# Kernel optimization log

Measured on AMD Instinct MI355X. Metric: run time of the kernel, lower is better.

The kernel has to match this reference:

```python
import jax, jax.numpy as jnp
import numpy as np

B, S, D_MODEL, H = 2, 2048, 1024, 16
HD = D_MODEL // H  # 64


def rotate_half(x):
    # pairs (x_even, x_odd) -> (-x_odd, x_even), interleaved back
    x1 = x[..., ::2]
    x2 = x[..., 1::2]
    return jnp.stack([-x2, x1], axis=-1).reshape(x.shape)


def rope_sin_cos(seq_len, head_dim):
    pos = jnp.arange(seq_len, dtype=jnp.float32)
    dim = jnp.arange(head_dim, dtype=jnp.float32)
    theta = 10000.0 ** (-2.0 * jnp.floor(dim / 2.0) / head_dim)
    angles = pos[:, None] * theta[None, :]  # [S, HD]
    return jnp.sin(angles), jnp.cos(angles)


def setup_inputs():
    key = jax.random.key(0)
    ks = jax.random.split(key, 6)
    w_scale = 1.0 / np.sqrt(D_MODEL)
    x = jax.random.normal(ks[0], (B, S, D_MODEL), jnp.float32)
    # causal mask: 1.0 where attention is disallowed (j > i)
    mask = (1.0 - jnp.tril(jnp.ones((S, S), jnp.float32)))[None, None, :, :]
    wq = jax.random.normal(ks[1], (D_MODEL, D_MODEL), jnp.float32) * w_scale
    wk = jax.random.normal(ks[2], (D_MODEL, D_MODEL), jnp.float32) * w_scale
    wv = jax.random.normal(ks[3], (D_MODEL, D_MODEL), jnp.float32) * w_scale
    wo = jax.random.normal(ks[4], (D_MODEL, D_MODEL), jnp.float32) * w_scale
    zeros = jnp.zeros((D_MODEL,), jnp.float32)
    return dict(x=x, mask=mask, wq=wq, bq=zeros, wk=wk, bk=zeros,
                wv=wv, bv=zeros, wo=wo, bo=zeros)


def reference(x, mask, wq, bq, wk, bk, wv, bv, wo, bo):
    b, s, _ = x.shape

    def split_heads(t):  # [B,S,D] -> [B,H,S,HD]
        return t.reshape(b, s, H, HD).transpose(0, 2, 1, 3)

    q = split_heads(x @ wq + bq)
    k = split_heads(x @ wk + bk)
    v = split_heads(x @ wv + bv)

    sin, cos = rope_sin_cos(s, HD)
    sin = sin[None, None, :, :]
    cos = cos[None, None, :, :]
    q = q * cos + rotate_half(q) * sin
    k = k * cos + rotate_half(k) * sin

    logits = jnp.einsum('bhqd,bhkd->bhqk', q, k) / jnp.sqrt(jnp.float32(HD))
    logits = logits + mask * (-1e9)
    attn = jax.nn.softmax(logits, axis=-1)
    out = jnp.einsum('bhqk,bhkd->bhqd', attn, v)  # [B,H,S,HD]
    out = out.transpose(0, 2, 1, 3).reshape(b, s, D_MODEL)
    return out @ wo + bo
```

## Files before the change

kernel.cpp:

```cpp
#include <hip/hip_runtime.h>
#include <hip/hip_bf16.h>


#define S_ 2048
#define DM 1024
#define HD 64

typedef __attribute__((ext_vector_type(8))) short short8;
typedef __attribute__((ext_vector_type(4))) float floatx4;

__device__ __forceinline__ unsigned short f2b(float x) {
  union { __hip_bfloat16 h; unsigned short u; } cv;
  cv.h = __float2bfloat16(x);
  return cv.u;
}

__device__ __forceinline__ unsigned cvt_pk_bf16(float lo, float hi) {
  unsigned r;
  asm("v_cvt_pk_bf16_f32 %0, %1, %2" : "=v"(r) : "v"(lo), "v"(hi));
  return r;
}

__device__ __forceinline__ void gload_lds16(const unsigned short* g, unsigned short* l) {
  typedef const __attribute__((address_space(1))) unsigned int* gp_t;
  typedef __attribute__((address_space(3))) unsigned int* lp_t;
  __builtin_amdgcn_global_load_lds((gp_t)(const void*)g, (lp_t)(void*)l, 16, 0, 0);
}

__global__ void prep_kernel(const float* __restrict__ x,
                            const float* __restrict__ w0, const float* __restrict__ w1,
                            const float* __restrict__ w2, const float* __restrict__ w3,
                            unsigned short* __restrict__ xc,
                            unsigned short* __restrict__ wt,
                            float2* __restrict__ rope) {
  const int bid = blockIdx.x;
  if (bid < 4096) {
    int i = (bid * 256 + threadIdx.x) * 4;
    float4 v = *(const float4*)(x + i);
    ushort4 o;
    o.x = f2b(v.x); o.y = f2b(v.y); o.z = f2b(v.z); o.w = f2b(v.w);
    *(ushort4*)(xc + i) = o;
  } else if (bid < 8192) {
    __shared__ float tile[32][33];
    const int rem = bid - 4096;
    const int z = rem >> 10;
    const int bx = (rem & 1023) & 31;
    const int by = (rem & 1023) >> 5;
    const float* W = (z == 0) ? w0 : (z == 1) ? w1 : (z == 2) ? w2 : w3;
    unsigned short* Wt = wt + (size_t)z * DM * DM;
    const int tx = threadIdx.x & 31;
    const int ty = threadIdx.x >> 5;
    const int k0 = bx * 32;
    const int c0 = by * 32;
#pragma unroll
    for (int i = 0; i < 4; ++i)
      tile[ty + i * 8][tx] = W[(size_t)(k0 + ty + i * 8) * DM + c0 + tx];
    __syncthreads();
#pragma unroll
    for (int i = 0; i < 4; ++i)
      Wt[(size_t)(c0 + ty + i * 8) * DM + k0 + tx] = f2b(tile[tx][ty + i * 8]);
  } else {
    int i = (bid - 8192) * 256 + threadIdx.x;
    int s = i >> 5, d2 = i & 31;
    float th = expf(-(float)d2 * (9.210340371976184f / 32.0f));
    float sn, cs;
    sincosf((float)s * th, &sn, &cs);
    rope[i] = make_float2(cs, sn);
  }
}

__global__ __launch_bounds__(256, 4) void gemm_qkv(
    const unsigned short* __restrict__ A, const unsigned short* __restrict__ Wt,
    const float* __restrict__ bq, const float* __restrict__ bk,
    const float* __restrict__ bv, const float2* __restrict__ rope,
    unsigned short* __restrict__ QKV) {
  __shared__ __attribute__((aligned(16))) unsigned short As[128 * 64];
  __shared__ __attribute__((aligned(16))) unsigned short Bs[64 * 64];
  const int r0 = blockIdx.x * 128;
  const int c0 = blockIdx.y * 64;
  const int t = threadIdx.x;
  const int lane = t & 63;
  const int wv = t >> 6;
  const int wr = (wv >> 1) * 64;
  const int wc = (wv & 1) * 32;
  const int lr = lane & 15;
  const int lg = lane >> 4;

  const int chunk = lane >> 3;
  const int sseg = ((lane & 7) ^ chunk) * 8;
  const unsigned short* Ag = A + (size_t)(r0 + wv * 32 + chunk) * DM + sseg;
  const unsigned short* Bg = Wt + (size_t)(c0 + wv * 16 + chunk) * DM + sseg;
  unsigned short* lA = &As[wv * 32 * 64];
  unsigned short* lB = &Bs[wv * 16 * 64];

  floatx4 acc[4][2] = {};
  const int fswz = (lr & 7) << 4;

  for (int k0 = 0; k0 < DM; k0 += 64) {
#pragma unroll
    for (int j = 0; j < 4; ++j)
      gload_lds16(Ag + k0 + j * 8 * DM, lA + j * 8 * 64);
#pragma unroll
    for (int j = 0; j < 2; ++j)
      gload_lds16(Bg + k0 + j * 8 * DM, lB + j * 8 * 64);
    __syncthreads();
#pragma unroll
    for (int kk = 0; kk < 2; ++kk) {
      short8 af[4], bf[2];
#pragma unroll
      for (int m = 0; m < 4; ++m)
        af[m] = *(const short8*)((char*)As + (wr + m * 16 + lr) * 128 +
                                 ((kk * 64 + lg * 16) ^ fswz));
#pragma unroll
      for (int n = 0; n < 2; ++n)
        bf[n] = *(const short8*)((char*)Bs + (wc + n * 16 + lr) * 128 +
                                 ((kk * 64 + lg * 16) ^ fswz));
#pragma unroll
      for (int m = 0; m < 4; ++m)
#pragma unroll
        for (int n = 0; n < 2; ++n)
          acc[m][n] = __builtin_amdgcn_mfma_f32_16x16x32_bf16(af[m], bf[n], acc[m][n], 0, 0, 0);
    }
    __syncthreads();
  }

  const int mat = blockIdx.y >> 4;
  const float* bias = (mat == 0) ? bq : (mat == 1) ? bk : bv;
  const int rbase = r0 + wr + lg * 4;
  const int cbase = c0 + wc + lr;
#pragma unroll
  for (int n = 0; n < 2; ++n) {
    const int c = cbase + n * 16;
    const int cc = c & (DM - 1);
    const float bvv = bias[cc];
    const int d = c & 63;
    const int h = cc >> 6;
#pragma unroll
    for (int m = 0; m < 4; ++m) {
#pragma unroll
      for (int i = 0; i < 4; ++i) {
        const int r = rbase + m * 16 + i;
        const int s = r & (S_ - 1);
        const int b = r >> 11;
        float v = acc[m][n][i] + bvv;
        float pv = __shfl_xor(v, 1);
        if (mat < 2) {
          float2 cssn = rope[s * 32 + (d >> 1)];
          v = (d & 1) ? fmaf(v, cssn.x, pv * cssn.y) : fmaf(v, cssn.x, -pv * cssn.y);
          if (mat == 0) v *= 0.18033688011112042f;
        }
        QKV[((size_t)((mat << 5) | (b << 4) | h) * S_ + s) * HD + d] = f2b(v);
      }
    }
  }
}

__global__ __launch_bounds__(256, 4) void gemm_out(
    const unsigned short* __restrict__ A, const unsigned short* __restrict__ Wt,
    const float* __restrict__ bias, float* __restrict__ out) {
  __shared__ __attribute__((aligned(16))) unsigned short As[64 * 64];
  __shared__ __attribute__((aligned(16))) unsigned short Bs[64 * 64];
  const int r0 = blockIdx.x * 64;
  const int c0 = blockIdx.y * 64;
  const int t = threadIdx.x;
  const int lane = t & 63;
  const int wv = t >> 6;
  const int wr = (wv >> 1) * 32;
  const int wc = (wv & 1) * 32;
  const int lr = lane & 15;
  const int lg = lane >> 4;

  const int chunk = lane >> 3;
  const int sseg = ((lane & 7) ^ chunk) * 8;
  const unsigned short* Ag = A + (size_t)(r0 + wv * 8 + chunk) * DM + sseg;
  const unsigned short* Bg = Wt + (size_t)(c0 + wv * 8 + chunk) * DM + sseg;
  unsigned short* lA = &As[wv * 8 * 64];
  unsigned short* lB = &Bs[wv * 8 * 64];

  floatx4 acc[2][2] = {};
  const int fswz = (lr & 7) << 4;

  for (int k0 = 0; k0 < DM; k0 += 64) {
#pragma unroll
    for (int j = 0; j < 2; ++j) {
      gload_lds16(Ag + k0 + j * 32 * DM, lA + j * 32 * 64);
      gload_lds16(Bg + k0 + j * 32 * DM, lB + j * 32 * 64);
    }
    __syncthreads();
#pragma unroll
    for (int kk = 0; kk < 2; ++kk) {
      short8 af[2], bf[2];
#pragma unroll
      for (int m = 0; m < 2; ++m)
        af[m] = *(const short8*)((char*)As + (wr + m * 16 + lr) * 128 +
                                 ((kk * 64 + lg * 16) ^ fswz));
#pragma unroll
      for (int n = 0; n < 2; ++n)
        bf[n] = *(const short8*)((char*)Bs + (wc + n * 16 + lr) * 128 +
                                 ((kk * 64 + lg * 16) ^ fswz));
#pragma unroll
      for (int m = 0; m < 2; ++m)
#pragma unroll
        for (int n = 0; n < 2; ++n)
          acc[m][n] = __builtin_amdgcn_mfma_f32_16x16x32_bf16(af[m], bf[n], acc[m][n], 0, 0, 0);
    }
    __syncthreads();
  }

  const int rbase = r0 + wr + lg * 4;
  const int cbase = c0 + wc + lr;
#pragma unroll
  for (int n = 0; n < 2; ++n) {
    const int c = cbase + n * 16;
    const float bvv = bias[c];
#pragma unroll
    for (int m = 0; m < 2; ++m) {
#pragma unroll
      for (int i = 0; i < 4; ++i) {
        const int r = rbase + m * 16 + i;
        out[(size_t)r * DM + c] = acc[m][n][i] + bvv;
      }
    }
  }
}

#define ATTN_STEP(TT, BUF, KLA, KLB)                                           \
  do {                                                                         \
    {                  \
      char* Vb = (char*)Vs[BUF];                                               \
      const unsigned* ua = (const unsigned*)&va;                               \
      const unsigned* ub = (const unsigned*)&vb;                               \
      _Pragma("unroll") for (int j = 0; j < 8; ++j) {                          \
        unsigned pkv = __builtin_amdgcn_perm(                                  \
            ub[j >> 1], ua[j >> 1], (j & 1) ? 0x07060302u : 0x05040100u);      \
        *(unsigned*)(Vb + (oct * 8 + j) * 128 + ((4 * kp) ^ (j << 4))) = pkv;  \
      }                                                                        \
    }                                                                          \
    if ((TT) < qt) {                                \
      va = *(const short8*)(Vpref);                                            \
      vb = *(const short8*)(Vpref + 64);                                       \
      Vpref += 4096;                                                           \
    }                                                                          \
                        \
    asm volatile("s_waitcnt lgkmcnt(0)" ::: "memory");                         \
    __builtin_amdgcn_s_barrier();                                              \
                 \
    if ((TT) < qt) asm volatile("s_waitcnt vmcnt(2)" ::: "memory");            \
    else           asm volatile("s_waitcnt vmcnt(0)" ::: "memory");            \
    __builtin_amdgcn_sched_barrier(0);                                         \
    if ((TT) < qt) {                   \
      gload_lds16(Kpref, KLA);                                                 \
      gload_lds16(Kpref + 2048, KLB);                                          \
      Kpref += 4096;                                                           \
    }                                                                          \
                     \
    floatx4 s[4] = {};                                                         \
    __builtin_amdgcn_s_setprio(1);                                             \
    _Pragma("unroll") for (int kk = 0; kk < 2; ++kk) {                         \
      _Pragma("unroll") for (int n = 0; n < 4; ++n) {                          \
        int r = n * 16 + lr;                                                   \
        short8 kf = *(const short8*)((char*)Ks[BUF] + r * 128 +                \
                                     ((kk * 64 + lg * 16) ^ ((r & 7) << 4)));  \
        s[n] = __builtin_amdgcn_mfma_f32_16x16x32_bf16(kf, qf[kk], s[n], 0, 0, 0); \
      }                                                                        \
    }                                                                          \
    __builtin_amdgcn_s_setprio(0);                                             \
    if ((TT) == qt) {                                                          \
      _Pragma("unroll") for (int n = 0; n < 4; ++n)                            \
        _Pragma("unroll") for (int i = 0; i < 4; ++i)                          \
          if (n * 16 + lg * 4 + i > qin) s[n][i] = -1e30f;                     \
    }                                                                          \
                              \
    float ta = fmaxf(fmaxf(s[0][0], s[0][1]), s[0][2]);                        \
    float tb = fmaxf(fmaxf(s[0][3], s[1][0]), s[1][1]);                        \
    float tc = fmaxf(fmaxf(s[1][2], s[1][3]), s[2][0]);                        \
    float td = fmaxf(fmaxf(s[2][1], s[2][2]), s[2][3]);                        \
    float te = fmaxf(fmaxf(s[3][0], s[3][1]), s[3][2]);                        \
    float tm = fmaxf(fmaxf(ta, tb), tc);                                       \
    tm = fmaxf(fmaxf(tm, td), te);                                             \
    tm = fmaxf(tm, s[3][3]);                                                   \
              \
    if (__any(tm > m + 8.f)) {                                                 \
      tm = fmaxf(tm, __shfl_xor(tm, 16));                                      \
      tm = fmaxf(tm, __shfl_xor(tm, 32));                                      \
      const float mn = fmaxf(m, tm);                                           \
      const float al = exp2f(m - mn);                                          \
      m = mn;                                                                  \
      lsum *= al;                                                              \
      _Pragma("unroll") for (int dd = 0; dd < 4; ++dd) o[dd] *= al;            \
    }                                                                          \
    float ps = 0.f;                                                            \
    _Pragma("unroll") for (int n = 0; n < 4; ++n) {                            \
      _Pragma("unroll") for (int i = 0; i < 4; ++i) {                          \
        float p = exp2f(s[n][i] - m);                                          \
        s[n][i] = p;                                                           \
        ps += p;                                                               \
      }                                                                        \
    }                                                                          \
    lsum += ps;                                                                \
                         \
    _Pragma("unroll") for (int n = 0; n < 4; ++n) {                            \
      _Pragma("unroll") for (int hh = 0; hh < 2; ++hh) {                       \
        unsigned pk = cvt_pk_bf16(s[n][2 * hh], s[n][2 * hh + 1]);             \
        *(unsigned*)(Pw + lr * 128 +                                           \
                     (((n * 16 + lg * 4 + 2 * hh) * 2) ^ pswz)) = pk;          \
      }                                                                        \
    }                                                                          \
    short8 pb[2];                                                              \
    _Pragma("unroll") for (int kk = 0; kk < 2; ++kk)                           \
      pb[kk] = *(const short8*)(Pw + lr * 128 + ((kk * 64 + lg * 16) ^ pswz)); \
    __builtin_amdgcn_s_setprio(1);                                             \
    _Pragma("unroll") for (int kk = 0; kk < 2; ++kk)                           \
      _Pragma("unroll") for (int dd = 0; dd < 4; ++dd) {                       \
        int d = dd * 16 + lr;                                                  \
        short8 vbf = *(const short8*)((char*)Vs[BUF] + d * 128 +               \
                                      ((kk * 64 + lg * 16) ^ ((d & 7) << 4))); \
        o[dd] = __builtin_amdgcn_mfma_f32_16x16x32_bf16(vbf, pb[kk], o[dd], 0, 0, 0); \
      }                                                                        \
    __builtin_amdgcn_s_setprio(0);                                             \
  } while (0)

__global__ __launch_bounds__(256, 4) void attn_kernel(
    const unsigned short* __restrict__ Q, const unsigned short* __restrict__ K,
    const unsigned short* __restrict__ V, unsigned short* __restrict__ AttnC) {
  __shared__ __attribute__((aligned(16))) unsigned short Ks[2][64 * 64];
  __shared__ __attribute__((aligned(16))) unsigned short Vs[2][64 * 64];
  __shared__ __attribute__((aligned(16))) unsigned short Ps[4][16 * 64];

  const int bh = blockIdx.x;
  const int qt = 31 - (int)blockIdx.y;
  const int tid = threadIdx.x;
  const int w = tid >> 6;
  const int l = tid & 63;
  const int lg = l >> 4;
  const int lr = l & 15;
  const size_t base = (size_t)bh * S_ * HD;
  const int qin = w * 16 + lr;

  short8 qf[2];
  {
    const unsigned short* Qrow =
        Q + base + (size_t)(qt * 64 + w * 16 + lr) * HD + lg * 8;
    qf[0] = *(const short8*)(Qrow);
    qf[1] = *(const short8*)(Qrow + 32);
  }

  floatx4 o[4] = {};
  float m = -1e30f, lsum = 0.f;

  const int krow = tid >> 3;
  const int kseg = tid & 7;
  const unsigned short* Kpref = K + base + krow * 64 + ((kseg ^ (krow & 7)) * 8);
  unsigned short* const kld0a = &Ks[0][w * 512];
  unsigned short* const kld0b = &Ks[0][2048 + w * 512];
  unsigned short* const kld1a = &Ks[1][w * 512];
  unsigned short* const kld1b = &Ks[1][2048 + w * 512];

  const int oct = tid >> 5;
  const int kp = tid & 31;
  const unsigned short* Vpref = V + base + 2 * kp * 64 + oct * 8;

  short8 va = *(const short8*)(Vpref);
  short8 vb = *(const short8*)(Vpref + 64);
  Vpref += 4096;
  gload_lds16(Kpref, kld0a);
  gload_lds16(Kpref + 2048, kld0b);
  Kpref += 4096;

  char* const Pw = (char*)Ps[w];
  const int pswz = (lr & 7) << 4;

  int t = 0;
#pragma unroll 1
  for (; t + 1 <= qt; t += 2) {
    ATTN_STEP(t, 0, kld1a, kld1b);
    ATTN_STEP(t + 1, 1, kld0a, kld0b);
  }
  if (t <= qt) ATTN_STEP(t, 0, kld1a, kld1b);

  lsum += __shfl_xor(lsum, 16);
  lsum += __shfl_xor(lsum, 32);
  const float inv = 1.f / lsum;
  unsigned short* orow =
      AttnC + (size_t)((bh >> 4) * S_ + qt * 64 + w * 16 + lr) * DM + (bh & 15) * HD;
#pragma unroll
  for (int dd = 0; dd < 4; ++dd) {
    unsigned w0 = cvt_pk_bf16(o[dd][0] * inv, o[dd][1] * inv);
    unsigned w1 = cvt_pk_bf16(o[dd][2] * inv, o[dd][3] * inv);
    *(uint2*)(orow + dd * 16 + lg * 4) = make_uint2(w0, w1);
  }
}

extern "C" void kernel_launch(void* const* d_in, const int* in_sizes, int n_in,
                              void* d_out, int out_size, void* d_ws, size_t ws_size,
                              hipStream_t stream) {
  const float* x = (const float*)d_in[0];
  const float* wq = (const float*)d_in[2];
  const float* bq = (const float*)d_in[3];
  const float* wk = (const float*)d_in[4];
  const float* bk = (const float*)d_in[5];
  const float* wv = (const float*)d_in[6];
  const float* bv = (const float*)d_in[7];
  const float* wo = (const float*)d_in[8];
  const float* bo = (const float*)d_in[9];

  char* ws = (char*)d_ws;
  const size_t MB = 1024ull * 1024ull;
  unsigned short* Xc = (unsigned short*)(ws);
  unsigned short* Wt = (unsigned short*)(ws + 8 * MB);
  unsigned short* QKVb = (unsigned short*)(ws + 16 * MB);
  unsigned short* Ac = (unsigned short*)(ws + 40 * MB);
  float2* rope = (float2*)(ws + 48 * MB);

  prep_kernel<<<8448, 256, 0, stream>>>(x, wq, wk, wv, wo, Xc, Wt, rope);
  gemm_qkv<<<dim3(32, 48), 256, 0, stream>>>(Xc, Wt, bq, bk, bv, rope, QKVb);
  attn_kernel<<<dim3(32, 32), 256, 0, stream>>>(
      QKVb, QKVb + 32ull * S_ * HD, QKVb + 64ull * S_ * HD, Ac);
  gemm_out<<<dim3(64, 16), 256, 0, stream>>>(Ac, Wt + 3ull * DM * DM, bo, (float*)d_out);
}
```

Before: 106.0 us.

## Write V transposed from QKV GEMM and load it via async LDS copies

The QKV GEMM epilogue for the V matrix now stages the tile in shared memory and writes V transposed ([b,h,d,s]) to a separate buffer. The attention kernel then fetches V^T tiles with direct global-to-LDS loads, the same way it fetches K, instead of loading V into registers and transposing it with byte permutes and LDS stores each step. This removes per-step register transposes and LDS write traffic in the attention inner loop. In exchange the GEMM epilogue gains an extra shared-memory pass and barrier, and the attention prologue now waits for the first tiles before entering the loop.

Measured after the change: 105.3 us, median of 2. About the same (-0.6%).

```diff
diff --git a/kernel.cpp b/kernel.cpp
--- a/kernel.cpp
+++ b/kernel.cpp
@@ -73,8 +73,8 @@
     const unsigned short* __restrict__ A, const unsigned short* __restrict__ Wt,
     const float* __restrict__ bq, const float* __restrict__ bk,
     const float* __restrict__ bv, const float2* __restrict__ rope,
-    unsigned short* __restrict__ QKV) {
-  __shared__ __attribute__((aligned(16))) unsigned short As[128 * 64];
+    unsigned short* __restrict__ QKV, unsigned short* __restrict__ VT) {
+  __shared__ __attribute__((aligned(16))) unsigned short As[64 * 136];
   __shared__ __attribute__((aligned(16))) unsigned short Bs[64 * 64];
   const int r0 = blockIdx.x * 128;
   const int c0 = blockIdx.y * 64;
@@ -128,28 +128,53 @@
   const float* bias = (mat == 0) ? bq : (mat == 1) ? bk : bv;
   const int rbase = r0 + wr + lg * 4;
   const int cbase = c0 + wc + lr;
-#pragma unroll
-  for (int n = 0; n < 2; ++n) {
-    const int c = cbase + n * 16;
-    const int cc = c & (DM - 1);
-    const float bvv = bias[cc];
-    const int d = c & 63;
-    const int h = cc >> 6;
-#pragma unroll
-    for (int m = 0; m < 4; ++m) {
-#pragma unroll
-      for (int i = 0; i < 4; ++i) {
-        const int r = rbase + m * 16 + i;
-        const int s = r & (S_ - 1);
-        const int b = r >> 11;
-        float v = acc[m][n][i] + bvv;
-        float pv = __shfl_xor(v, 1);
-        if (mat < 2) {
+
+  if (mat == 2) {
+    unsigned short* Ls = As;
+#pragma unroll
+    for (int n = 0; n < 2; ++n) {
+      const int dl = wc + n * 16 + lr;
+      const float bvv = bias[(c0 & (DM - 1)) + dl];
+#pragma unroll
+      for (int m = 0; m < 4; ++m)
+#pragma unroll
+        for (int i = 0; i < 4; ++i)
+          Ls[dl * 136 + (wr + m * 16 + lg * 4 + i)] = f2b(acc[m][n][i] + bvv);
+    }
+    __syncthreads();
+    const int b2 = r0 >> 11;
+    const int h2 = (c0 & (DM - 1)) >> 6;
+    const int s0 = r0 & (S_ - 1);
+    unsigned short* VTb = VT + ((size_t)((b2 << 4) | h2) * 64) * S_ + s0;
+#pragma unroll
+    for (int j = 0; j < 4; ++j) {
+      const int idx = t + j * 256;
+      const int d = idx >> 4;
+      const int sg = idx & 15;
+      *(int4*)(VTb + (size_t)d * S_ + sg * 8) = *(const int4*)(Ls + d * 136 + sg * 8);
+    }
+  } else {
+#pragma unroll
+    for (int n = 0; n < 2; ++n) {
+      const int c = cbase + n * 16;
+      const int cc = c & (DM - 1);
+      const float bvv = bias[cc];
+      const int d = c & 63;
+      const int h = cc >> 6;
+#pragma unroll
+      for (int m = 0; m < 4; ++m) {
+#pragma unroll
+        for (int i = 0; i < 4; ++i) {
+          const int r = rbase + m * 16 + i;
+          const int s = r & (S_ - 1);
+          const int b = r >> 11;
+          float v = acc[m][n][i] + bvv;
+          float pv = __shfl_xor(v, 1);
           float2 cssn = rope[s * 32 + (d >> 1)];
           v = (d & 1) ? fmaf(v, cssn.x, pv * cssn.y) : fmaf(v, cssn.x, -pv * cssn.y);
           if (mat == 0) v *= 0.18033688011112042f;
+          QKV[((size_t)((mat << 5) | (b << 4) | h) * S_ + s) * HD + d] = f2b(v);
         }
-        QKV[((size_t)((mat << 5) | (b << 4) | h) * S_ + s) * HD + d] = f2b(v);
       }
     }
   }
@@ -224,36 +249,23 @@
   }
 }
 
-#define ATTN_STEP(TT, BUF, KLA, KLB)                                           \
+#define ATTN_STEP(TT, BUF, KLA, KLB, VLA, VLB)                                 \
   do {                                                                         \
-    {                  \
-      char* Vb = (char*)Vs[BUF];                                               \
-      const unsigned* ua = (const unsigned*)&va;                               \
-      const unsigned* ub = (const unsigned*)&vb;                               \
-      _Pragma("unroll") for (int j = 0; j < 8; ++j) {                          \
-        unsigned pkv = __builtin_amdgcn_perm(                                  \
-            ub[j >> 1], ua[j >> 1], (j & 1) ? 0x07060302u : 0x05040100u);      \
-        *(unsigned*)(Vb + (oct * 8 + j) * 128 + ((4 * kp) ^ (j << 4))) = pkv;  \
-      }                                                                        \
-    }                                                                          \
-    if ((TT) < qt) {                                \
-      va = *(const short8*)(Vpref);                                            \
-      vb = *(const short8*)(Vpref + 64);                                       \
-      Vpref += 4096;                                                           \
-    }                                                                          \
-                        \
     asm volatile("s_waitcnt lgkmcnt(0)" ::: "memory");                         \
     __builtin_amdgcn_s_barrier();                                              \
-                 \
-    if ((TT) < qt) asm volatile("s_waitcnt vmcnt(2)" ::: "memory");            \
-    else           asm volatile("s_waitcnt vmcnt(0)" ::: "memory");            \
-    __builtin_amdgcn_sched_barrier(0);                                         \
-    if ((TT) < qt) {                   \
+    if ((TT) < qt) {                        \
       gload_lds16(Kpref, KLA);                                                 \
       gload_lds16(Kpref + 2048, KLB);                                          \
+      gload_lds16(VTpref, VLA);                                                \
+      gload_lds16(VTpref + 32 * S_, VLB);                                      \
       Kpref += 4096;                                                           \
-    }                                                                          \
-                     \
+      VTpref += 64;                                                            \
+      asm volatile("s_waitcnt vmcnt(4)" ::: "memory");                         \
+    } else {                                                                   \
+      asm volatile("s_waitcnt vmcnt(0)" ::: "memory");                         \
+    }                                                                          \
+    __builtin_amdgcn_sched_barrier(0);                                         \
+                         \
     floatx4 s[4] = {};                                                         \
     __builtin_amdgcn_s_setprio(1);                                             \
     _Pragma("unroll") for (int kk = 0; kk < 2; ++kk) {                         \
@@ -322,7 +334,7 @@
 
 __global__ __launch_bounds__(256, 4) void attn_kernel(
     const unsigned short* __restrict__ Q, const unsigned short* __restrict__ K,
-    const unsigned short* __restrict__ V, unsigned short* __restrict__ AttnC) {
+    const unsigned short* __restrict__ VT, unsigned short* __restrict__ AttnC) {
   __shared__ __attribute__((aligned(16))) unsigned short Ks[2][64 * 64];
   __shared__ __attribute__((aligned(16))) unsigned short Vs[2][64 * 64];
   __shared__ __attribute__((aligned(16))) unsigned short Ps[4][16 * 64];
@@ -351,21 +363,25 @@
   const int krow = tid >> 3;
   const int kseg = tid & 7;
   const unsigned short* Kpref = K + base + krow * 64 + ((kseg ^ (krow & 7)) * 8);
+  const unsigned short* VTpref =
+      VT + ((size_t)bh * 64 + krow) * S_ + ((kseg ^ (krow & 7)) * 8);
   unsigned short* const kld0a = &Ks[0][w * 512];
   unsigned short* const kld0b = &Ks[0][2048 + w * 512];
   unsigned short* const kld1a = &Ks[1][w * 512];
   unsigned short* const kld1b = &Ks[1][2048 + w * 512];
-
-  const int oct = tid >> 5;
-  const int kp = tid & 31;
-  const unsigned short* Vpref = V + base + 2 * kp * 64 + oct * 8;
-
-  short8 va = *(const short8*)(Vpref);
-  short8 vb = *(const short8*)(Vpref + 64);
-  Vpref += 4096;
+  unsigned short* const vld0a = &Vs[0][w * 512];
+  unsigned short* const vld0b = &Vs[0][2048 + w * 512];
+  unsigned short* const vld1a = &Vs[1][w * 512];
+  unsigned short* const vld1b = &Vs[1][2048 + w * 512];
+
   gload_lds16(Kpref, kld0a);
   gload_lds16(Kpref + 2048, kld0b);
+  gload_lds16(VTpref, vld0a);
+  gload_lds16(VTpref + 32 * S_, vld0b);
   Kpref += 4096;
+  VTpref += 64;
+  asm volatile("s_waitcnt vmcnt(0)" ::: "memory");
+  __builtin_amdgcn_s_barrier();
 
   char* const Pw = (char*)Ps[w];
   const int pswz = (lr & 7) << 4;
@@ -373,10 +389,10 @@
   int t = 0;
 #pragma unroll 1
   for (; t + 1 <= qt; t += 2) {
-    ATTN_STEP(t, 0, kld1a, kld1b);
-    ATTN_STEP(t + 1, 1, kld0a, kld0b);
-  }
-  if (t <= qt) ATTN_STEP(t, 0, kld1a, kld1b);
+    ATTN_STEP(t, 0, kld1a, kld1b, vld1a, vld1b);
+    ATTN_STEP(t + 1, 1, kld0a, kld0b, vld0a, vld0b);
+  }
+  if (t <= qt) ATTN_STEP(t, 0, kld1a, kld1b, vld1a, vld1b);
 
   lsum += __shfl_xor(lsum, 16);
   lsum += __shfl_xor(lsum, 32);
@@ -409,12 +425,13 @@
   unsigned short* Xc = (unsigned short*)(ws);
   unsigned short* Wt = (unsigned short*)(ws + 8 * MB);
   unsigned short* QKVb = (unsigned short*)(ws + 16 * MB);
+  unsigned short* VTb = (unsigned short*)(ws + 32 * MB);
   unsigned short* Ac = (unsigned short*)(ws + 40 * MB);
   float2* rope = (float2*)(ws + 48 * MB);
 
   prep_kernel<<<8448, 256, 0, stream>>>(x, wq, wk, wv, wo, Xc, Wt, rope);
-  gemm_qkv<<<dim3(32, 48), 256, 0, stream>>>(Xc, Wt, bq, bk, bv, rope, QKVb);
+  gemm_qkv<<<dim3(32, 48), 256, 0, stream>>>(Xc, Wt, bq, bk, bv, rope, QKVb, VTb);
   attn_kernel<<<dim3(32, 32), 256, 0, stream>>>(
-      QKVb, QKVb + 32ull * S_ * HD, QKVb + 64ull * S_ * HD, Ac);
+      QKVb, QKVb + 32ull * S_ * HD, VTb, Ac);
   gemm_out<<<dim3(64, 16), 256, 0, stream>>>(Ac, Wt + 3ull * DM * DM, bo, (float*)d_out);
 }
```
